# Optimization experiments

Hardware: AMD Instinct MI355X
Metric: run time of the kernel (lower is better)

The kernel has to match this reference:

```python
import jax, jax.numpy as jnp
import numpy as np

ALPHA = 0.2  # LeakyReLU negative slope

def setup_inputs() -> dict:
    key = jax.random.key(0)
    k1, k2, k3, k4 = jax.random.split(key, 4)
    N, F_in, F_out = 8192, 512, 64
    x = jax.random.normal(k1, (N, F_in), dtype=jnp.float32)
    adj = jax.random.randint(k2, (N, N), 0, 2, dtype=jnp.int32)
    # xavier-normal-ish init
    weight = jax.random.normal(k3, (F_in, F_out), dtype=jnp.float32) * np.sqrt(2.0 / (F_in + F_out))
    a = jax.random.normal(k4, (2 * F_out, 1), dtype=jnp.float32) * np.sqrt(2.0 / (2 * F_out + 1))
    return {"x": x, "adj": adj, "weight": weight, "a": a}

def reference(x, adj, weight, a):
    # Wh: [N, F_out]
    Wh = x @ weight
    F_out = weight.shape[1]
    a1 = a[:F_out, 0]   # applies to source (row) node
    a2 = a[F_out:, 0]   # applies to target (col) node
    # e[i,j] = LeakyReLU(Wh[i]@a1 + Wh[j]@a2)  -- broadcast-add instead of O(N^2*2F) concat
    s1 = Wh @ a1        # [N]
    s2 = Wh @ a2        # [N]
    e = s1[:, None] + s2[None, :]              # [N, N]
    e = jnp.where(e > 0, e, ALPHA * e)         # LeakyReLU
    e = jnp.where(adj > 0, e, jnp.float32(-9e15))
    attention = jax.nn.softmax(e, axis=1)      # [N, N]
    h_prime = attention @ Wh                   # [N, F_out]
    return jax.nn.elu(h_prime)                 # concat=True -> ELU
```

## Files before the change

### kernel.cpp

```cpp
#include <hip/hip_runtime.h>
#include <hip/hip_bf16.h>
#include <cstdint>
#include <cstddef>

#define N_NODES 8192
#define F_IN 512
#define F_OUT 64
#define LOG2E 1.44269504f

#define JSPLIT 8
#define JPB (N_NODES / JSPLIT)
#define JC 256
#define NCHUNK (JPB / JC)

typedef __attribute__((ext_vector_type(8))) short short8v;
typedef __attribute__((ext_vector_type(4))) float f32x4;
typedef __attribute__((ext_vector_type(4))) int i32x4;
typedef __attribute__((ext_vector_type(4))) unsigned int u32x4;

static __device__ __forceinline__ unsigned short f2bf(float f) {
    union { float f; unsigned u; } v; v.f = f;
    unsigned u = v.u + 0x7FFFu + ((v.u >> 16) & 1u);
    return (unsigned short)(u >> 16);
}
static __device__ __forceinline__ float bf2f(unsigned short b) {
    union { unsigned u; float f; } v; v.u = ((unsigned)b) << 16;
    return v.f;
}
static __device__ __forceinline__ unsigned cvt_pk_bf16(float lo, float hi) {
    unsigned r;
    asm("v_cvt_pk_bf16_f32 %0, %1, %2" : "=v"(r) : "v"(lo), "v"(hi));
    return r;
}

__global__ __launch_bounds__(256)
void gat_pack(const int* __restrict__ adj, unsigned char* __restrict__ mask) {
    const unsigned t = blockIdx.x * 256 + threadIdx.x;
    const size_t stride = (size_t)2048 * 256;
    #pragma unroll 4
    for (int it = 0; it < 16; ++it) {
        const size_t b = (size_t)it * stride + t;
        const i32x4* p = (const i32x4*)(adj + b * 8);
        i32x4 v0 = p[0], v1 = p[1];
        unsigned byte =  (v0[0] & 1)        | ((v0[1] & 1) << 1)
                      | ((v0[2] & 1) << 2)  | ((v0[3] & 1) << 3)
                      | ((v1[0] & 1) << 4)  | ((v1[1] & 1) << 5)
                      | ((v1[2] & 1) << 6)  | ((v1[3] & 1) << 7);
        mask[b] = (unsigned char)byte;
    }
}

__global__ __launch_bounds__(256)
void gat_wconv(const float* __restrict__ W, unsigned short* __restrict__ whf,
               unsigned short* __restrict__ wlf) {
    const int t = blockIdx.x * 256 + threadIdx.x;
    const int tile = t >> 6, lane = t & 63;
    const int kt = tile >> 2, ct = tile & 3;
    const int k0 = kt * 32 + ((lane >> 4) << 3);
    const int c  = ct * 16 + (lane & 15);
    short8v h, l;
    #pragma unroll
    for (int i = 0; i < 8; ++i) {
        float v = W[(size_t)(k0 + i) * F_OUT + c];
        unsigned short hb = f2bf(v);
        h[i] = (short)hb;
        l[i] = (short)f2bf(v - bf2f(hb));
    }
    const size_t dst = (size_t)tile * 512 + (size_t)lane * 8;
    *(short8v*)(whf + dst) = h;
    *(short8v*)(wlf + dst) = l;
}

__global__ __launch_bounds__(256)
void gat_prep(const float* __restrict__ x, const unsigned short* __restrict__ whf,
              const unsigned short* __restrict__ wlf, const float* __restrict__ a,
              unsigned short* __restrict__ whtf,
              float* __restrict__ s1, float* __restrict__ s2) {
    __shared__ f32x4 red[2][4][64];
    __shared__ unsigned short ldsT[64][40];
    const int tid = threadIdx.x;
    const int lane = tid & 63;
    const int wv = tid >> 6;
    const int rt = wv & 1;
    const int kh = wv >> 1;
    const int l15 = lane & 15, g = lane >> 4;
    const int jt = blockIdx.x;
    const int row0 = jt * 32 + rt * 16;

    f32x4 acc[4] = {{0.f,0.f,0.f,0.f},{0.f,0.f,0.f,0.f},{0.f,0.f,0.f,0.f},{0.f,0.f,0.f,0.f}};

    const float* xp = x + (size_t)(row0 + l15) * F_IN + kh * 256 + g * 8;
    float4 v[16];
    #pragma unroll
    for (int q = 0; q < 8; ++q) {
        v[2 * q]     = *(const float4*)(xp + q * 32);
        v[2 * q + 1] = *(const float4*)(xp + q * 32 + 4);
    }
    #pragma unroll
    for (int q = 0; q < 8; ++q) {
        const int kt = kh * 8 + q;
        float vv[8] = {v[2*q].x, v[2*q].y, v[2*q].z, v[2*q].w,
                       v[2*q+1].x, v[2*q+1].y, v[2*q+1].z, v[2*q+1].w};
        short8v xh, xl;
        #pragma unroll
        for (int i = 0; i < 8; ++i) {
            unsigned short hb = f2bf(vv[i]);
            xh[i] = (short)hb;
            xl[i] = (short)f2bf(vv[i] - bf2f(hb));
        }
        const unsigned short* wp = whf + (size_t)(kt * 4) * 512 + (size_t)lane * 8;
        const unsigned short* lp = wlf + (size_t)(kt * 4) * 512 + (size_t)lane * 8;
        #pragma unroll
        for (int ct = 0; ct < 4; ++ct) {
            short8v wh = *(const short8v*)(wp + ct * 512);
            short8v wl = *(const short8v*)(lp + ct * 512);
            acc[ct] = __builtin_amdgcn_mfma_f32_16x16x32_bf16(xh, wh, acc[ct], 0, 0, 0);
            acc[ct] = __builtin_amdgcn_mfma_f32_16x16x32_bf16(xl, wh, acc[ct], 0, 0, 0);
            acc[ct] = __builtin_amdgcn_mfma_f32_16x16x32_bf16(xh, wl, acc[ct], 0, 0, 0);
        }
    }

    if (kh == 1) {
        #pragma unroll
        for (int ct = 0; ct < 4; ++ct) red[rt][ct][lane] = acc[ct];
    }
    __syncthreads();

    if (kh == 0) {
        #pragma unroll
        for (int ct = 0; ct < 4; ++ct) acc[ct] += red[rt][ct][lane];

        #pragma unroll
        for (int r = 0; r < 4; ++r) {
            float p1 = 0.f, p2 = 0.f;
            #pragma unroll
            for (int ct = 0; ct < 4; ++ct) {
                p1 = fmaf(acc[ct][r], a[ct * 16 + l15], p1);
                p2 = fmaf(acc[ct][r], a[64 + ct * 16 + l15], p2);
            }
            p1 += __shfl_xor(p1, 1); p2 += __shfl_xor(p2, 1);
            p1 += __shfl_xor(p1, 2); p2 += __shfl_xor(p2, 2);
            p1 += __shfl_xor(p1, 4); p2 += __shfl_xor(p2, 4);
            p1 += __shfl_xor(p1, 8); p2 += __shfl_xor(p2, 8);
            if (l15 == 0) {
                s1[row0 + g * 4 + r] = p1 * LOG2E;
                s2[row0 + g * 4 + r] = p2 * LOG2E;
            }
        }

        #pragma unroll
        for (int ct = 0; ct < 4; ++ct) {
            ushort4 pk;
            pk.x = f2bf(acc[ct][0]); pk.y = f2bf(acc[ct][1]);
            pk.z = f2bf(acc[ct][2]); pk.w = f2bf(acc[ct][3]);
            *(ushort4*)&ldsT[ct * 16 + l15][rt * 16 + g * 4] = pk;
        }
    }
    __syncthreads();

    {
        const int jb = jt >> 2, gj = jt & 3;
        const int m  = tid >> 6;
        const int ct = (tid >> 4) & 3;
        const int c  = tid & 15;
        short8v sv = *(const short8v*)&ldsT[ct * 16 + c][m * 8];
        *(short8v*)(whtf + (size_t)jb * 8192 + m * 2048 + ct * 512
                         + (size_t)(gj * 16 + c) * 8) = sv;
    }
}

__global__ __launch_bounds__(512, 4)
void gat_main(const unsigned char* __restrict__ mask, const unsigned short* __restrict__ whtf,
              const float* __restrict__ s1, const float* __restrict__ s2,
              float* __restrict__ numpart, float* __restrict__ denpart) {
    __shared__ unsigned short lds[2][JC * F_OUT];
    const int tid  = threadIdx.x;
    const int lane = tid & 63;
    const int wv   = tid >> 6;
    const int l15  = lane & 15, g = lane >> 4;
    const int rg   = blockIdx.x >> 3;
    const int js   = blockIdx.x & 7;
    const int rowbase = rg * 128 + wv * 16;
    const int row  = rowbase + l15;
    const int j0   = js * JPB;
    const float s1r = s1[row];

    const char* gbase = (const char*)whtf + (size_t)j0 * 128;
    const unsigned* mrow = (const unsigned*)mask + (size_t)row * (N_NODES / 32) + (j0 >> 5) + g;
    const float* s2b = s2 + j0 + g * 32;

    f32x4 acc0 = {0.f, 0.f, 0.f, 0.f};
    f32x4 acc1 = acc0, acc2 = acc0, acc3 = acc0;
    float dsum = 0.f;

    #define STAGE(ch, buf) do { \
        const char* _g = gbase + (size_t)(ch) * 32768 + (size_t)tid * 16; \
        char* _l = (char*)&lds[buf][0] + (size_t)wv * 1024; \
        _Pragma("unroll") \
        for (int _i = 0; _i < 4; ++_i) \
            __builtin_amdgcn_global_load_lds( \
                (const __attribute__((address_space(1))) void*)(_g + _i * 8192), \
                (__attribute__((address_space(3))) void*)(_l + _i * 8192), 16, 0, 0); \
    } while (0)

    STAGE(0, 0);
    __syncthreads();

    for (int ch = 0; ch < NCHUNK; ++ch) {
        const int cur = ch & 1;
        if (ch < NCHUNK - 1) STAGE(ch + 1, cur ^ 1);

        const unsigned short* lbuf = &lds[cur][0];
        #pragma unroll
        for (int h = 0; h < 2; ++h) {
            const int jbl = ch * 2 + h;
            const unsigned mw = mrow[jbl * 4];
            const unsigned short* gb = lbuf + h * 8192;
            #pragma unroll
            for (int q = 0; q < 4; ++q) {
                const unsigned mb = (mw >> (q * 8)) & 0xffu;
                const int jw = jbl * 128 + q * 8;
                float4 sa = *(const float4*)(s2b + jw);
                float4 sb = *(const float4*)(s2b + jw + 4);

                short8v b0 = *(const short8v*)(gb + q * 2048 +    0 + lane * 8);
                short8v b1 = *(const short8v*)(gb + q * 2048 +  512 + lane * 8);
                short8v b2 = *(const short8v*)(gb + q * 2048 + 1024 + lane * 8);
                short8v b3 = *(const short8v*)(gb + q * 2048 + 1536 + lane * 8);

                float w0, w1, w2, w3, w4, w5, w6, w7;
                #define GAT_EL(wvar, bi, s2v) do { \
                    float e = s1r + (s2v); e = fmaxf(e, 0.2f * e); \
                    float ex = __builtin_amdgcn_exp2f(e); \
                    wvar = ((mb >> (bi)) & 1u) ? ex : 0.f; dsum += wvar; } while (0);
                GAT_EL(w0, 0, sa.x) GAT_EL(w1, 1, sa.y)
                GAT_EL(w2, 2, sa.z) GAT_EL(w3, 3, sa.w)
                GAT_EL(w4, 4, sb.x) GAT_EL(w5, 5, sb.y)
                GAT_EL(w6, 6, sb.z) GAT_EL(w7, 7, sb.w)
                #undef GAT_EL

                u32x4 au;
                au[0] = cvt_pk_bf16(w0, w1);
                au[1] = cvt_pk_bf16(w2, w3);
                au[2] = cvt_pk_bf16(w4, w5);
                au[3] = cvt_pk_bf16(w6, w7);
                short8v afrag = __builtin_bit_cast(short8v, au);

                acc0 = __builtin_amdgcn_mfma_f32_16x16x32_bf16(afrag, b0, acc0, 0, 0, 0);
                acc1 = __builtin_amdgcn_mfma_f32_16x16x32_bf16(afrag, b1, acc1, 0, 0, 0);
                acc2 = __builtin_amdgcn_mfma_f32_16x16x32_bf16(afrag, b2, acc2, 0, 0, 0);
                acc3 = __builtin_amdgcn_mfma_f32_16x16x32_bf16(afrag, b3, acc3, 0, 0, 0);
            }
        }
        __syncthreads();
    }
    #undef STAGE

    dsum += __shfl_xor(dsum, 16);
    dsum += __shfl_xor(dsum, 32);
    if (lane < 16) denpart[(size_t)js * N_NODES + rowbase + lane] = dsum;

    float* np = numpart + ((size_t)js * N_NODES + rowbase) * F_OUT;
    #pragma unroll
    for (int r = 0; r < 4; ++r) {
        const int ro = (g * 4 + r) * F_OUT;
        np[ro +  0 + l15] = acc0[r];
        np[ro + 16 + l15] = acc1[r];
        np[ro + 32 + l15] = acc2[r];
        np[ro + 48 + l15] = acc3[r];
    }
}

__global__ __launch_bounds__(256)
void gat_combine(const float* __restrict__ numpart, const float* __restrict__ denpart,
                 float* __restrict__ out) {
    const int idx = blockIdx.x * 256 + threadIdx.x;
    const int r = idx >> 6;
    float num = 0.f, den = 0.f;
    #pragma unroll
    for (int c = 0; c < JSPLIT; ++c) {
        num += numpart[(size_t)c * N_NODES * F_OUT + idx];
        den += denpart[(size_t)c * N_NODES + r];
    }
    float h = num / den;
    out[idx] = h > 0.f ? h : __expf(h) - 1.f;
}

extern "C" void kernel_launch(void* const* d_in, const int* in_sizes, int n_in,
                              void* d_out, int out_size, void* d_ws, size_t ws_size,
                              hipStream_t stream) {
    const float* x      = (const float*)d_in[0];
    const int*   adj    = (const int*)d_in[1];
    const float* weight = (const float*)d_in[2];
    const float* a      = (const float*)d_in[3];
    float* out = (float*)d_out;

    char* ws = (char*)d_ws;
    unsigned short* whtf = (unsigned short*)ws;
    float* s1            = (float*)(ws + 1048576);
    float* s2            = (float*)(ws + 1048576 + 32768);
    unsigned short* whf  = (unsigned short*)(ws + 1048576 + 65536);
    unsigned short* wlf  = (unsigned short*)(ws + 1048576 + 131072);
    float* numpart       = (float*)(ws + 1245184);
    float* denpart       = (float*)(ws + 1245184 + 16777216);
    unsigned char* mask  = (unsigned char*)(ws + 1245184 + 16777216 + 262144);

    gat_pack<<<2048, 256, 0, stream>>>(adj, mask);
    gat_wconv<<<16, 256, 0, stream>>>(weight, whf, wlf);
    gat_prep<<<N_NODES / 32, 256, 0, stream>>>(x, whf, wlf, a, whtf, s1, s2);
    gat_main<<<64 * JSPLIT, 512, 0, stream>>>(mask, whtf, s1, s2, numpart, denpart);
    gat_combine<<<N_NODES * F_OUT / 256, 256, 0, stream>>>(numpart, denpart, out);
}
```

Measured before the change: 100.7 us.

## Fuse adjacency bit-packing into main attention kernel via register prefetch and LDS

```diff
diff --git a/kernel.cpp b/kernel.cpp
--- a/kernel.cpp
+++ b/kernel.cpp
@@ -31,23 +31,6 @@
     unsigned r;
     asm("v_cvt_pk_bf16_f32 %0, %1, %2" : "=v"(r) : "v"(lo), "v"(hi));
     return r;
-}
-
-__global__ __launch_bounds__(256)
-void gat_pack(const int* __restrict__ adj, unsigned char* __restrict__ mask) {
-    const unsigned t = blockIdx.x * 256 + threadIdx.x;
-    const size_t stride = (size_t)2048 * 256;
-    #pragma unroll 4
-    for (int it = 0; it < 16; ++it) {
-        const size_t b = (size_t)it * stride + t;
-        const i32x4* p = (const i32x4*)(adj + b * 8);
-        i32x4 v0 = p[0], v1 = p[1];
-        unsigned byte =  (v0[0] & 1)        | ((v0[1] & 1) << 1)
-                      | ((v0[2] & 1) << 2)  | ((v0[3] & 1) << 3)
-                      | ((v1[0] & 1) << 4)  | ((v1[1] & 1) << 5)
-                      | ((v1[2] & 1) << 6)  | ((v1[3] & 1) << 7);
-        mask[b] = (unsigned char)byte;
-    }
 }
 
 __global__ __launch_bounds__(256)
@@ -169,11 +152,12 @@
     }
 }
 
-__global__ __launch_bounds__(512, 4)
-void gat_main(const unsigned char* __restrict__ mask, const unsigned short* __restrict__ whtf,
+__global__ __launch_bounds__(512)
+void gat_main(const int* __restrict__ adj, const unsigned short* __restrict__ whtf,
               const float* __restrict__ s1, const float* __restrict__ s2,
               float* __restrict__ numpart, float* __restrict__ denpart) {
     __shared__ unsigned short lds[2][JC * F_OUT];
+    __shared__ unsigned char mlds[8][16][68];
     const int tid  = threadIdx.x;
     const int lane = tid & 63;
     const int wv   = tid >> 6;
@@ -186,12 +170,13 @@
     const float s1r = s1[row];
 
     const char* gbase = (const char*)whtf + (size_t)j0 * 128;
-    const unsigned* mrow = (const unsigned*)mask + (size_t)row * (N_NODES / 32) + (j0 >> 5) + g;
+    const int*  astage = adj + (size_t)rowbase * N_NODES + j0;
     const float* s2b = s2 + j0 + g * 32;
 
     f32x4 acc0 = {0.f, 0.f, 0.f, 0.f};
     f32x4 acc1 = acc0, acc2 = acc0, acc3 = acc0;
     float dsum = 0.f;
+    i32x4 areg[16];
 
     #define STAGE(ch, buf) do { \
         const char* _g = gbase + (size_t)(ch) * 32768 + (size_t)tid * 16; \
@@ -203,23 +188,41 @@
                 (__attribute__((address_space(3))) void*)(_l + _i * 8192), 16, 0, 0); \
     } while (0)
 
+    #define LOADA(ch) do { \
+        _Pragma("unroll") \
+        for (int _r = 0; _r < 16; ++_r) \
+            areg[_r] = *(const i32x4*)(astage + (size_t)_r * N_NODES + (ch) * 256 + lane * 4); \
+    } while (0)
+
+    #define PACKW() do { \
+        _Pragma("unroll") \
+        for (int _r = 0; _r < 16; ++_r) { \
+            i32x4 _v = areg[_r]; \
+            unsigned _nib = ((unsigned)_v[0] & 1u) | (((unsigned)_v[1] & 1u) << 1) \
+                          | (((unsigned)_v[2] & 1u) << 2) | (((unsigned)_v[3] & 1u) << 3); \
+            mlds[wv][_r][lane] = (unsigned char)_nib; \
+        } \
+    } while (0)
+
     STAGE(0, 0);
+    LOADA(0);
     __syncthreads();
+    PACKW();
 
     for (int ch = 0; ch < NCHUNK; ++ch) {
         const int cur = ch & 1;
-        if (ch < NCHUNK - 1) STAGE(ch + 1, cur ^ 1);
+        if (ch < NCHUNK - 1) { STAGE(ch + 1, cur ^ 1); LOADA(ch + 1); }
 
         const unsigned short* lbuf = &lds[cur][0];
         #pragma unroll
         for (int h = 0; h < 2; ++h) {
-            const int jbl = ch * 2 + h;
-            const unsigned mw = mrow[jbl * 4];
             const unsigned short* gb = lbuf + h * 8192;
             #pragma unroll
             for (int q = 0; q < 4; ++q) {
-                const unsigned mb = (mw >> (q * 8)) & 0xffu;
-                const int jw = jbl * 128 + q * 8;
+                const unsigned short w16 =
+                    *(const unsigned short*)&mlds[wv][l15][h * 32 + g * 8 + q * 2];
+                const unsigned mb = (w16 & 0xfu) | ((w16 >> 4) & 0xf0u);
+                const int jw = (ch * 2 + h) * 128 + q * 8;
                 float4 sa = *(const float4*)(s2b + jw);
                 float4 sb = *(const float4*)(s2b + jw + 4);
 
@@ -253,8 +256,11 @@
             }
         }
         __syncthreads();
+        if (ch < NCHUNK - 1) PACKW();
     }
     #undef STAGE
+    #undef LOADA
+    #undef PACKW
 
     dsum += __shfl_xor(dsum, 16);
     dsum += __shfl_xor(dsum, 32);
@@ -303,11 +309,9 @@
     unsigned short* wlf  = (unsigned short*)(ws + 1048576 + 131072);
     float* numpart       = (float*)(ws + 1245184);
     float* denpart       = (float*)(ws + 1245184 + 16777216);
-    unsigned char* mask  = (unsigned char*)(ws + 1245184 + 16777216 + 262144);
-
-    gat_pack<<<2048, 256, 0, stream>>>(adj, mask);
+
     gat_wconv<<<16, 256, 0, stream>>>(weight, whf, wlf);
     gat_prep<<<N_NODES / 32, 256, 0, stream>>>(x, whf, wlf, a, whtf, s1, s2);
-    gat_main<<<64 * JSPLIT, 512, 0, stream>>>(mask, whtf, s1, s2, numpart, denpart);
+    gat_main<<<64 * JSPLIT, 512, 0, stream>>>(adj, whtf, s1, s2, numpart, denpart);
     gat_combine<<<N_NODES * F_OUT / 256, 256, 0, stream>>>(numpart, denpart, out);
 }
```

New measurement: 101.2 us. Within noise of the previous version (+0.5%).
